# Kernel tuning notes

Measured on AMD Instinct MI355X. Metric: run time of the kernel, lower is better.

Reference implementation:

```python
import jax, jax.numpy as jnp
import numpy as np

B, N, C, H = 32, 4096, 768, 12
D = C // H  # head dim
SCALE = D ** -0.5


def setup_inputs() -> dict:
    key = jax.random.key(0)
    ks = jax.random.split(key, 5)
    s = C ** -0.5
    return {
        "x": jax.random.normal(ks[0], (B, N, C), dtype=jnp.float32),
        "Wq": jax.random.normal(ks[1], (C, C), dtype=jnp.float32) * s,
        "Wkv": jax.random.normal(ks[2], (C, 2 * C), dtype=jnp.float32) * s,
        "Wp": jax.random.normal(ks[3], (C, C), dtype=jnp.float32) * s,
        "bp": jax.random.normal(ks[4], (C,), dtype=jnp.float32) * 0.01,
    }


def reference(x, Wq, Wkv, Wp, bp):
    b, n, c = x.shape
    h, d = H, c // H
    # single CLS query: [B,1,C] -> [B,H,1,d], pre-scaled
    q = (x[:, :1, :] @ Wq).reshape(b, 1, h, d).transpose(0, 2, 1, 3) * SCALE
    kv = (x @ Wkv).reshape(b, n, 2, h, d).transpose(2, 0, 3, 1, 4)
    k, v = kv[0], kv[1]
    # scores [B,H,1,N] -> softmax over N -> weighted V sum [B,H,1,d]
    attn = jax.nn.softmax(jnp.einsum("bhqd,bhnd->bhqn", q, k), axis=-1)
    cls = jnp.einsum("bhqn,bhnd->bhqd", attn, v).transpose(0, 2, 1, 3).reshape(b, 1, c)
    return cls @ Wp + bp
```

## Files before the change

### kernel.cpp

```cpp
#include <hip/hip_runtime.h>

#define B 32
#define N 4096
#define C 768
#define H 12
#define D 64
#define SCALE 0.125f
#define CH 16
#define NT 256
#define TILE 8
#define NTILE 32

typedef __attribute__((ext_vector_type(4))) float f4;

__global__ __launch_bounds__(256)
void k_q(const float* __restrict__ x, const float* __restrict__ Wq,
         float* __restrict__ q){
  int b = blockIdx.x, jb = blockIdx.y, tid = threadIdx.x;
  __shared__ float xs[C];
  for (int c = tid; c < C; c += 256) xs[c] = x[(size_t)b*N*C + c];
  __syncthreads();
  int j = jb*256 + tid;
  float acc = 0.f;
  #pragma unroll 8
  for (int c = 0; c < C; ++c) acc += xs[c] * Wq[(size_t)c*C + j];
  q[(size_t)b*C + j] = acc;
}

__global__ __launch_bounds__(256)
void k_r(const float* __restrict__ q, const float* __restrict__ Wkv,
         float* __restrict__ r){
  int b = blockIdx.x, h = blockIdx.y;
  int tid = threadIdx.x, w = tid >> 6, lane = tid & 63;
  float qv = q[(size_t)b*C + h*D + lane] * SCALE;
  for (int c = w; c < C; c += 4){
    float wv = Wkv[(size_t)c*(2*C) + h*D + lane];
    float p = qv * wv;
    #pragma unroll
    for (int m = 1; m < 64; m <<= 1) p += __shfl_xor(p, m, 64);
    if (lane == 0) r[((size_t)b*H + h)*C + c] = p;
  }
}

__global__ __launch_bounds__(256)
void k_fused(const float* __restrict__ x, const float* __restrict__ r,
             float* __restrict__ pm, float* __restrict__ pl,
             float* __restrict__ pxb){
  int b = blockIdx.x, ch = blockIdx.y;
  int tid = threadIdx.x, w = tid >> 6, lane = tid & 63;

  __shared__ float xs[TILE][C];
  __shared__ float scr[TILE][H][20];
  __shared__ float sc[TILE][16];
  __shared__ float wts[TILE][16];
  __shared__ float als[16];

  f4 rr4[3][3];
  {
    const float* rb = r + ((size_t)b*H + 3*w)*C + 4*lane;
    #pragma unroll
    for (int hh = 0; hh < 3; ++hh)
      #pragma unroll
      for (int jj = 0; jj < 3; ++jj)
        rr4[hh][jj] = *(const f4*)(rb + hh*C + 256*jj);
  }

  float m0 = -1e30f, l0 = 0.f;
  float xb[H][3];
  #pragma unroll
  for (int h = 0; h < H; ++h){ xb[h][0]=0.f; xb[h][1]=0.f; xb[h][2]=0.f; }

  const float* gx = x + ((size_t)b*N + (size_t)ch*NT)*C;
  f4 pf[6];
  #pragma unroll
  for (int k = 0; k < 6; ++k) pf[k] = ((const f4*)gx)[tid + 256*k];

  for (int tt = 0; tt < NTILE; ++tt){
    f4* xd = (f4*)&xs[0][0];
    #pragma unroll
    for (int k = 0; k < 6; ++k) xd[tid + 256*k] = pf[k];
    if (tt + 1 < NTILE){
      const f4* gn = (const f4*)(gx + (size_t)(tt+1)*TILE*C);
      #pragma unroll
      for (int k = 0; k < 6; ++k) pf[k] = gn[tid + 256*k];
    }
    __syncthreads();

    float acc[TILE][3];
    #pragma unroll
    for (int t = 0; t < TILE; ++t){ acc[t][0]=0.f; acc[t][1]=0.f; acc[t][2]=0.f; }
    #pragma unroll
    for (int t = 0; t < TILE; ++t){
      f4 p0 = *(const f4*)&xs[t][4*lane];
      f4 p1 = *(const f4*)&xs[t][4*lane + 256];
      f4 p2 = *(const f4*)&xs[t][4*lane + 512];
      #pragma unroll
      for (int hh = 0; hh < 3; ++hh){
        f4 r0 = rr4[hh][0], r1 = rr4[hh][1], r2 = rr4[hh][2];
        acc[t][hh] += p0.x*r0.x + p0.y*r0.y + p0.z*r0.z + p0.w*r0.w
                    + p1.x*r1.x + p1.y*r1.y + p1.z*r1.z + p1.w*r1.w
                    + p2.x*r2.x + p2.y*r2.y + p2.z*r2.z + p2.w*r2.w;
      }
    }
    #pragma unroll
    for (int t = 0; t < TILE; ++t)
      #pragma unroll
      for (int hh = 0; hh < 3; ++hh){
        acc[t][hh] += __shfl_xor(acc[t][hh], 32, 64);
        acc[t][hh] += __shfl_xor(acc[t][hh], 16, 64);
      }
    if (lane < 16){
      #pragma unroll
      for (int t = 0; t < TILE; ++t)
        #pragma unroll
        for (int hh = 0; hh < 3; ++hh)
          scr[t][3*w + hh][lane] = acc[t][hh];
    }
    __syncthreads();

    if (tid < 96){
      int t8 = tid & 7, h12 = tid >> 3;
      float s = 0.f;
      #pragma unroll
      for (int qq = 0; qq < 4; ++qq){
        f4 v = *(const f4*)&scr[t8][h12][4*qq];
        s += v.x + v.y + v.z + v.w;
      }
      sc[t8][h12] = s;
    }
    __syncthreads();

    if (tid < H){
      float tm = sc[0][tid];
      #pragma unroll
      for (int t = 1; t < TILE; ++t) tm = fmaxf(tm, sc[t][tid]);
      float mnew = fmaxf(m0, tm);
      float alpha = __expf(m0 - mnew);
      float wsum = 0.f;
      #pragma unroll
      for (int t = 0; t < TILE; ++t){
        float wv = __expf(sc[t][tid] - mnew);
        wts[t][tid] = wv;
        wsum += wv;
      }
      l0 = l0*alpha + wsum;
      m0 = mnew;
      als[tid] = alpha;
    }
    __syncthreads();

    f4 av0 = *(const f4*)&als[0];
    f4 av1 = *(const f4*)&als[4];
    f4 av2 = *(const f4*)&als[8];
    float alf[H] = {av0.x,av0.y,av0.z,av0.w, av1.x,av1.y,av1.z,av1.w,
                    av2.x,av2.y,av2.z,av2.w};
    #pragma unroll
    for (int h = 0; h < H; ++h){
      xb[h][0] *= alf[h]; xb[h][1] *= alf[h]; xb[h][2] *= alf[h];
    }
    #pragma unroll
    for (int t = 0; t < TILE; ++t){
      f4 w0 = *(const f4*)&wts[t][0];
      f4 w1 = *(const f4*)&wts[t][4];
      f4 w2 = *(const f4*)&wts[t][8];
      float wf[H] = {w0.x,w0.y,w0.z,w0.w, w1.x,w1.y,w1.z,w1.w,
                     w2.x,w2.y,w2.z,w2.w};
      float x0 = xs[t][tid], x1 = xs[t][tid+256], x2 = xs[t][tid+512];
      #pragma unroll
      for (int h = 0; h < H; ++h){
        xb[h][0] += wf[h]*x0;
        xb[h][1] += wf[h]*x1;
        xb[h][2] += wf[h]*x2;
      }
    }
    __syncthreads();
  }

  size_t pbase = ((size_t)b*CH + ch)*H;
  if (tid < H){ pm[pbase + tid] = m0; pl[pbase + tid] = l0; }
  #pragma unroll
  for (int h = 0; h < H; ++h){
    size_t o = (pbase + h)*C + tid;
    pxb[o]       = xb[h][0];
    pxb[o + 256] = xb[h][1];
    pxb[o + 512] = xb[h][2];
  }
}

__global__ __launch_bounds__(256)
void k_cls(const float* __restrict__ pm, const float* __restrict__ pl,
           const float* __restrict__ pxb, const float* __restrict__ Wkv,
           float* __restrict__ cls){
  int b = blockIdx.x, h = blockIdx.y, tid = threadIdx.x;
  __shared__ float xsm[C];
  float M = -1e30f;
  #pragma unroll
  for (int c = 0; c < CH; ++c) M = fmaxf(M, pm[((size_t)b*CH + c)*H + h]);
  float L = 0.f;
  float eh[CH];
  #pragma unroll
  for (int c = 0; c < CH; ++c){
    eh[c] = __expf(pm[((size_t)b*CH + c)*H + h] - M);
    L += pl[((size_t)b*CH + c)*H + h]*eh[c];
  }
  float inv = 1.f/L;
  #pragma unroll
  for (int k = 0; k < 3; ++k){
    int c = tid + 256*k;
    float acc = 0.f;
    #pragma unroll
    for (int q = 0; q < CH; ++q)
      acc += eh[q]*pxb[(((size_t)b*CH + q)*H + h)*C + c];
    xsm[c] = acc*inv;
  }
  __syncthreads();
  int d = tid & 63, part = tid >> 6;
  float acc = 0.f;
  int c0 = part*192;
  #pragma unroll 4
  for (int cc = c0; cc < c0 + 192; ++cc)
    acc += xsm[cc]*Wkv[(size_t)cc*(2*C) + C + h*D + d];
  __shared__ float red[4][D];
  red[part][d] = acc; __syncthreads();
  if (tid < D)
    cls[(size_t)b*C + h*D + tid] = red[0][tid]+red[1][tid]+red[2][tid]+red[3][tid];
}

__global__ __launch_bounds__(256)
void k_out(const float* __restrict__ cls, const float* __restrict__ Wp,
           const float* __restrict__ bp, float* __restrict__ out){
  int b = blockIdx.x, jb = blockIdx.y, tid = threadIdx.x;
  __shared__ float xs[C];
  for (int i = tid; i < C; i += 256) xs[i] = cls[(size_t)b*C + i];
  __syncthreads();
  int j = jb*256 + tid;
  float acc = bp[j];
  #pragma unroll 4
  for (int i = 0; i < C; ++i) acc += xs[i]*Wp[(size_t)i*C + j];
  out[(size_t)b*C + j] = acc;
}

extern "C" void kernel_launch(void* const* d_in, const int* in_sizes, int n_in,
                              void* d_out, int out_size, void* d_ws, size_t ws_size,
                              hipStream_t stream){
  const float* x   = (const float*)d_in[0];
  const float* Wq  = (const float*)d_in[1];
  const float* Wkv = (const float*)d_in[2];
  const float* Wp  = (const float*)d_in[3];
  const float* bp  = (const float*)d_in[4];
  float* out = (float*)d_out;
  char* ws = (char*)d_ws;
  float* q   = (float*)(ws + 0);
  float* r   = (float*)(ws + 98304);
  float* pm  = (float*)(ws + 1277952);
  float* pl  = (float*)(ws + 1302528);
  float* pxb = (float*)(ws + 1327104);
  float* cls = (float*)(ws + 20201472);

  k_q    <<<dim3(B,3),  dim3(256), 0, stream>>>(x, Wq, q);
  k_r    <<<dim3(B,H),  dim3(256), 0, stream>>>(q, Wkv, r);
  k_fused<<<dim3(B,CH), dim3(256), 0, stream>>>(x, r, pm, pl, pxb);
  k_cls  <<<dim3(B,H),  dim3(256), 0, stream>>>(pm, pl, pxb, Wkv, cls);
  k_out  <<<dim3(B,3),  dim3(256), 0, stream>>>(cls, Wp, bp, out);
}
```

Before: 882.4 us.

## Fuse q and r projection kernels and double sequence split count

Merges the q projection into the r kernel so each (batch, head) block computes only its 64 q values, which removes one launch and the q round trip through global memory. Doubles the number of sequence chunks in the fused attention kernel (32 chunks of 128 tokens) so more blocks run, for better occupancy across CUs. Splits the score accumulation into two halves of four tokens to lower register pressure. In exchange the partial xb buffer doubles in size and the combine kernel has more partials to read.

Result: faster. 854.2 us (-3.2%).

```diff
diff --git a/kernel.cpp b/kernel.cpp
--- a/kernel.cpp
+++ b/kernel.cpp
@@ -6,33 +6,34 @@
 #define H 12
 #define D 64
 #define SCALE 0.125f
-#define CH 16
-#define NT 256
+#define CH 32
+#define NT 128
 #define TILE 8
-#define NTILE 32
+#define NTILE 16
 
 typedef __attribute__((ext_vector_type(4))) float f4;
 
 __global__ __launch_bounds__(256)
-void k_q(const float* __restrict__ x, const float* __restrict__ Wq,
-         float* __restrict__ q){
-  int b = blockIdx.x, jb = blockIdx.y, tid = threadIdx.x;
-  __shared__ float xs[C];
-  for (int c = tid; c < C; c += 256) xs[c] = x[(size_t)b*N*C + c];
-  __syncthreads();
-  int j = jb*256 + tid;
-  float acc = 0.f;
-  #pragma unroll 8
-  for (int c = 0; c < C; ++c) acc += xs[c] * Wq[(size_t)c*C + j];
-  q[(size_t)b*C + j] = acc;
-}
-
-__global__ __launch_bounds__(256)
-void k_r(const float* __restrict__ q, const float* __restrict__ Wkv,
-         float* __restrict__ r){
+void k_qr(const float* __restrict__ x, const float* __restrict__ Wq,
+          const float* __restrict__ Wkv, float* __restrict__ r){
   int b = blockIdx.x, h = blockIdx.y;
   int tid = threadIdx.x, w = tid >> 6, lane = tid & 63;
-  float qv = q[(size_t)b*C + h*D + lane] * SCALE;
+  __shared__ float xs[C];
+  __shared__ float qred[4][D];
+  __shared__ float qs[D];
+  for (int c = tid; c < C; c += 256) xs[c] = x[(size_t)b*N*C + c];
+  __syncthreads();
+  float acc = 0.f;
+  int c0 = w*192;
+  #pragma unroll 4
+  for (int cc = c0; cc < c0+192; ++cc)
+    acc += xs[cc]*Wq[(size_t)cc*C + h*D + lane];
+  qred[w][lane] = acc;
+  __syncthreads();
+  if (tid < D)
+    qs[tid] = (qred[0][tid]+qred[1][tid]+qred[2][tid]+qred[3][tid])*SCALE;
+  __syncthreads();
+  float qv = qs[lane];
   for (int c = w; c < C; c += 4){
     float wv = Wkv[(size_t)c*(2*C) + h*D + lane];
     float p = qv * wv;
@@ -86,35 +87,39 @@
     }
     __syncthreads();
 
-    float acc[TILE][3];
-    #pragma unroll
-    for (int t = 0; t < TILE; ++t){ acc[t][0]=0.f; acc[t][1]=0.f; acc[t][2]=0.f; }
-    #pragma unroll
-    for (int t = 0; t < TILE; ++t){
-      f4 p0 = *(const f4*)&xs[t][4*lane];
-      f4 p1 = *(const f4*)&xs[t][4*lane + 256];
-      f4 p2 = *(const f4*)&xs[t][4*lane + 512];
-      #pragma unroll
-      for (int hh = 0; hh < 3; ++hh){
-        f4 r0 = rr4[hh][0], r1 = rr4[hh][1], r2 = rr4[hh][2];
-        acc[t][hh] += p0.x*r0.x + p0.y*r0.y + p0.z*r0.z + p0.w*r0.w
-                    + p1.x*r1.x + p1.y*r1.y + p1.z*r1.z + p1.w*r1.w
-                    + p2.x*r2.x + p2.y*r2.y + p2.z*r2.z + p2.w*r2.w;
-      }
-    }
-    #pragma unroll
-    for (int t = 0; t < TILE; ++t)
-      #pragma unroll
-      for (int hh = 0; hh < 3; ++hh){
-        acc[t][hh] += __shfl_xor(acc[t][hh], 32, 64);
-        acc[t][hh] += __shfl_xor(acc[t][hh], 16, 64);
-      }
-    if (lane < 16){
-      #pragma unroll
-      for (int t = 0; t < TILE; ++t)
+    #pragma unroll
+    for (int hf = 0; hf < 2; ++hf){
+      float acc[4][3];
+      #pragma unroll
+      for (int t4 = 0; t4 < 4; ++t4){ acc[t4][0]=0.f; acc[t4][1]=0.f; acc[t4][2]=0.f; }
+      #pragma unroll
+      for (int t4 = 0; t4 < 4; ++t4){
+        int t = hf*4 + t4;
+        f4 p0 = *(const f4*)&xs[t][4*lane];
+        f4 p1 = *(const f4*)&xs[t][4*lane + 256];
+        f4 p2 = *(const f4*)&xs[t][4*lane + 512];
         #pragma unroll
-        for (int hh = 0; hh < 3; ++hh)
-          scr[t][3*w + hh][lane] = acc[t][hh];
+        for (int hh = 0; hh < 3; ++hh){
+          f4 r0 = rr4[hh][0], r1 = rr4[hh][1], r2 = rr4[hh][2];
+          acc[t4][hh] += p0.x*r0.x + p0.y*r0.y + p0.z*r0.z + p0.w*r0.w
+                       + p1.x*r1.x + p1.y*r1.y + p1.z*r1.z + p1.w*r1.w
+                       + p2.x*r2.x + p2.y*r2.y + p2.z*r2.z + p2.w*r2.w;
+        }
+      }
+      #pragma unroll
+      for (int t4 = 0; t4 < 4; ++t4)
+        #pragma unroll
+        for (int hh = 0; hh < 3; ++hh){
+          acc[t4][hh] += __shfl_xor(acc[t4][hh], 32, 64);
+          acc[t4][hh] += __shfl_xor(acc[t4][hh], 16, 64);
+        }
+      if (lane < 16){
+        #pragma unroll
+        for (int t4 = 0; t4 < 4; ++t4)
+          #pragma unroll
+          for (int hh = 0; hh < 3; ++hh)
+            scr[hf*4 + t4][3*w + hh][lane] = acc[t4][hh];
+      }
     }
     __syncthreads();
 
@@ -208,7 +213,7 @@
   for (int k = 0; k < 3; ++k){
     int c = tid + 256*k;
     float acc = 0.f;
-    #pragma unroll
+    #pragma unroll 8
     for (int q = 0; q < CH; ++q)
       acc += eh[q]*pxb[(((size_t)b*CH + q)*H + h)*C + c];
     xsm[c] = acc*inv;
@@ -250,15 +255,13 @@
   const float* bp  = (const float*)d_in[4];
   float* out = (float*)d_out;
   char* ws = (char*)d_ws;
-  float* q   = (float*)(ws + 0);
-  float* r   = (float*)(ws + 98304);
-  float* pm  = (float*)(ws + 1277952);
-  float* pl  = (float*)(ws + 1302528);
-  float* pxb = (float*)(ws + 1327104);
-  float* cls = (float*)(ws + 20201472);
-
-  k_q    <<<dim3(B,3),  dim3(256), 0, stream>>>(x, Wq, q);
-  k_r    <<<dim3(B,H),  dim3(256), 0, stream>>>(q, Wkv, r);
+  float* r   = (float*)(ws + 0);
+  float* pm  = (float*)(ws + 1179648);
+  float* pl  = (float*)(ws + 1228800);
+  float* pxb = (float*)(ws + 1277952);
+  float* cls = (float*)(ws + 39026688);
+
+  k_qr   <<<dim3(B,H),  dim3(256), 0, stream>>>(x, Wq, Wkv, r);
   k_fused<<<dim3(B,CH), dim3(256), 0, stream>>>(x, r, pm, pl, pxb);
   k_cls  <<<dim3(B,H),  dim3(256), 0, stream>>>(pm, pl, pxb, Wkv, cls);
   k_out  <<<dim3(B,3),  dim3(256), 0, stream>>>(cls, Wp, bp, out);
```
